# Optimization experiments

Hardware: AMD Instinct MI355X
Metric: run time of the kernel (lower is better)

Reference implementation:

```python
import jax, jax.numpy as jnp
import numpy as np

B, S, E, H = 8, 1024, 1024, 16
D = E // H  # per-head dim = 64
STD = 0.05  # nn.init.normal_ std used in the torch module


def setup_inputs() -> dict:
    key = jax.random.key(0)
    ks = jax.random.split(key, 9)
    inputs = jax.random.normal(ks[0], (B, S, E), dtype=jnp.float32)
    mlp_params_Q = jax.random.normal(ks[1], (B, E), dtype=jnp.float32)
    mlp_params_K = jax.random.normal(ks[2], (B, E), dtype=jnp.float32)
    W_Query = jax.random.normal(ks[3], (E, E), dtype=jnp.float32) * STD
    W_Key = jax.random.normal(ks[4], (E, E), dtype=jnp.float32) * STD
    W_Value = jax.random.normal(ks[5], (E, E), dtype=jnp.float32) * STD
    W_Out = jax.random.normal(ks[6], (E, E), dtype=jnp.float32) * STD  # nn.Linear weight [out, in]
    ln_gamma = jax.random.normal(ks[7], (E,), dtype=jnp.float32) * STD
    ln_beta = jax.random.normal(ks[8], (E,), dtype=jnp.float32) * STD
    return {"inputs": inputs, "mlp_params_Q": mlp_params_Q, "mlp_params_K": mlp_params_K,
            "W_Query": W_Query, "W_Key": W_Key, "W_Value": W_Value, "W_Out": W_Out,
            "ln_gamma": ln_gamma, "ln_beta": ln_beta}


def reference(inputs, mlp_params_Q, mlp_params_K, W_Query, W_Key, W_Value, W_Out, ln_gamma, ln_beta):
    # QKV projections: [B,S,E] @ [E,E]
    q = jnp.einsum('bse,ef->bsf', inputs, W_Query)
    k = jnp.einsum('bse,ef->bsf', inputs, W_Key)
    v = jnp.einsum('bse,ef->bsf', inputs, W_Value)
    # meta gate modulation (flag='gate', mode='QK'): per-batch channel gates, *2
    q = q * mlp_params_Q[:, None, :] * 2.0
    k = k * mlp_params_K[:, None, :] * 2.0
    # split heads: channels [h*D:(h+1)*D] -> head h (matches torch.split/stack)
    qh = q.reshape(B, S, H, D)
    kh = k.reshape(B, S, H, D)
    vh = v.reshape(B, S, H, D)
    # attention scores [B,H,S,S], scaled by sqrt(D)
    scores = jnp.einsum('bihd,bjhd->bhij', qh, kh) / jnp.sqrt(jnp.asarray(D, q.dtype))
    attn = jax.nn.softmax(scores, axis=-1)  # attn_dropout is identity at eval
    out = jnp.einsum('bhij,bjhd->bihd', attn, vh).reshape(B, S, E)  # concat heads
    # output projection (nn.Linear, no bias): x @ W.T; dropout identity at eval
    res = jnp.einsum('bse,fe->bsf', out, W_Out)
    # residual + LayerNorm(eps=1e-6)
    res = res + inputs
    mean = jnp.mean(res, axis=-1, keepdims=True)
    var = jnp.mean(jnp.square(res - mean), axis=-1, keepdims=True)
    res = (res - mean) * jax.lax.rsqrt(var + 1e-6) * ln_gamma + ln_beta
    return res
```

## Files before the change

kernel.cpp:

```cpp
#include <hip/hip_runtime.h>
#include <stdint.h>

#define Bn 8
#define Sn 1024
#define En 1024
#define Hn 16
#define Dn 64
#define Mn (Bn*Sn)

typedef unsigned short u16;
typedef _Float16 f16;
typedef _Float16 f16x8 __attribute__((ext_vector_type(8)));
typedef __fp16   h16x2 __attribute__((ext_vector_type(2)));
typedef float    f32x4 __attribute__((ext_vector_type(4)));

static __device__ __forceinline__ u16 f2h(float x){
  f16 h = (f16)x;
  union { f16 h; u16 u; } c; c.h = h; return c.u;
}
static __device__ __forceinline__ float h2f(u16 u){
  union { u16 u; f16 h; } c; c.u = u; return (float)c.h;
}
static __device__ __forceinline__ float fexp2(float x){
  float r; asm("v_exp_f32 %0, %1" : "=v"(r) : "v"(x)); return r;
}
static __device__ __forceinline__ f32x4 mfma16(f16x8 a, f16x8 b, f32x4 c){
  return __builtin_amdgcn_mfma_f32_16x16x32_f16(a, b, c, 0, 0, 0);
}
static __device__ __forceinline__ void gl_lds16(const u16* g, u16* l){
  __builtin_amdgcn_global_load_lds((__attribute__((address_space(1))) void*)g,
                                   (__attribute__((address_space(3))) void*)l, 16, 0, 0);
}

__global__ __launch_bounds__(256) void k_prep(const float* __restrict__ X,
    const float* __restrict__ Wq, const float* __restrict__ Wk,
    const float* __restrict__ Wv, const float* __restrict__ Wo,
    u16* __restrict__ xh, u16* __restrict__ wq, u16* __restrict__ wk,
    u16* __restrict__ wv, u16* __restrict__ wo){
  __shared__ float tsh[32][33];
  const int bid = blockIdx.x, tid = threadIdx.x;
  if (bid < 9216){
    const float* src = (bid < 8192) ? X : Wo;
    u16* dst = (bid < 8192) ? xh : wo;
    int i = (bid < 8192 ? bid : bid - 8192)*256 + tid;
    float4 v = ((const float4*)src)[i];
    ushort4 h; h.x = f2h(v.x); h.y = f2h(v.y); h.z = f2h(v.z); h.w = f2h(v.w);
    ((ushort4*)dst)[i] = h;
  } else {
    int pb = bid - 9216;
    int sel = pb >> 10, inner = pb & 1023;
    int bx = inner & 31, by = inner >> 5;
    int tx = tid & 31, ty = tid >> 5;
    const float* W = (sel == 0) ? Wq : (sel == 1) ? Wk : Wv;
    u16* D = (sel == 0) ? wq : (sel == 1) ? wk : wv;
    for (int i = 0; i < 32; i += 8)
      tsh[ty+i][tx] = W[(size_t)(by*32+ty+i)*En + bx*32+tx];
    __syncthreads();
    for (int i = 0; i < 32; i += 8)
      D[(size_t)(bx*32+ty+i)*En + by*32+tx] = f2h(tsh[tx][ty+i]);
  }
}

__global__ __launch_bounds__(256) void k_gemm_qkv(
    const u16* __restrict__ A, const u16* __restrict__ Bw,
    const float* __restrict__ gQ, const float* __restrict__ gK,
    u16* __restrict__ Cq, u16* __restrict__ Ck, u16* __restrict__ Vt){
  __shared__ u16 sA[2*128*32], sB[2*128*32];
  const int t = threadIdx.x, w = t >> 6, l = t & 63;
  const int lr = l & 15, lg = l >> 4;
  const int tn = blockIdx.x % 24, tm = blockIdx.x / 24;
  const int m0 = tm*128, n0 = tn*128;
  const int wr = (w >> 1)*64, wc = (w & 1)*64;
  f32x4 acc[4][4] = {};

#define GSTAGE(buf, k0_) do { \
    for (int c = 0; c < 2; c++){ \
      int ch  = c*256 + t; \
      int row = ch >> 2; \
      int xb  = (ch & 3) << 4; \
      int col = (k0_) + ((xb ^ ((row & 3) << 4)) >> 1); \
      int ldso = (buf)*8192 + (c*256 + w*64)*16; \
      gl_lds16(A  + (size_t)(m0+row)*En + col, (u16*)((char*)sA + ldso)); \
      gl_lds16(Bw + (size_t)(n0+row)*En + col, (u16*)((char*)sB + ldso)); \
    } } while (0)

  GSTAGE(0, 0);
  __syncthreads();
  for (int kt = 0; kt < En/32; kt++){
    const int cur = kt & 1;
    if (kt < En/32 - 1) GSTAGE(cur^1, (kt+1)*32);
    f16x8 af[4], bf[4];
    #pragma unroll
    for (int i = 0; i < 4; i++){
      int r  = wr + i*16 + lr;
      af[i] = *(const f16x8*)((const char*)sA + cur*8192 + r*64 + ((lg*16) ^ ((r & 3) << 4)));
      int n  = wc + i*16 + lr;
      bf[i] = *(const f16x8*)((const char*)sB + cur*8192 + n*64 + ((lg*16) ^ ((n & 3) << 4)));
    }
    __builtin_amdgcn_s_setprio(1);
    #pragma unroll
    for (int i = 0; i < 4; i++)
      #pragma unroll
      for (int j = 0; j < 4; j++)
        acc[i][j] = mfma16(af[i], bf[j], acc[i][j]);
    __builtin_amdgcn_s_setprio(0);
    __syncthreads();
  }
#undef GSTAGE
  const int bb = m0 >> 10;
  const int sel = n0 >> 10;
  if (sel < 2){
    const float* gate = sel ? gK : gQ;
    const float gs = sel ? 2.0f : 0.25f*1.4426950408889634f;
    u16* C = sel ? Ck : Cq;
    #pragma unroll
    for (int j = 0; j < 4; j++){
      int col = (n0 & 1023) + wc + j*16 + lr;
      float g = gate[bb*En + col] * gs;
      #pragma unroll
      for (int i = 0; i < 4; i++){
        int mbase = m0 + wr + i*16 + lg*4;
        #pragma unroll
        for (int r = 0; r < 4; r++)
          C[(size_t)(mbase + r)*En + col] = f2h(acc[i][j][r] * g);
      }
    }
  } else {
    const int s0 = (m0 & 1023) + wr;
    #pragma unroll
    for (int j = 0; j < 4; j++){
      int nn = (n0 - 2048) + wc + j*16 + lr;
      int hh = nn >> 6, d = nn & 63;
      u16* dst = Vt + ((size_t)(bb*Hn + hh)*Dn + d)*Sn;
      #pragma unroll
      for (int i = 0; i < 4; i++){
        int ss = s0 + i*16 + lg*4;
        ushort4 pk;
        pk.x = f2h(acc[i][j][0]); pk.y = f2h(acc[i][j][1]);
        pk.z = f2h(acc[i][j][2]); pk.w = f2h(acc[i][j][3]);
        *(ushort4*)&dst[ss] = pk;
      }
    }
  }
}

__global__ __launch_bounds__(256) void k_gemm_out(
    const u16* __restrict__ A, const u16* __restrict__ Bw,
    const float* __restrict__ resid, u16* __restrict__ resh){
  __shared__ u16 sA[2*128*32], sB[2*128*32];
  const int t = threadIdx.x, w = t >> 6, l = t & 63;
  const int lr = l & 15, lg = l >> 4;
  const int tn = blockIdx.x & 7, tm = blockIdx.x >> 3;
  const int m0 = tm*128, n0 = tn*128;
  const int wr = (w >> 1)*64, wc = (w & 1)*64;
  f32x4 acc[4][4] = {};

#define GSTAGE(buf, k0_) do { \
    for (int c = 0; c < 2; c++){ \
      int ch  = c*256 + t; \
      int row = ch >> 2; \
      int xb  = (ch & 3) << 4; \
      int col = (k0_) + ((xb ^ ((row & 3) << 4)) >> 1); \
      int ldso = (buf)*8192 + (c*256 + w*64)*16; \
      gl_lds16(A  + (size_t)(m0+row)*En + col, (u16*)((char*)sA + ldso)); \
      gl_lds16(Bw + (size_t)(n0+row)*En + col, (u16*)((char*)sB + ldso)); \
    } } while (0)

  GSTAGE(0, 0);
  __syncthreads();
  for (int kt = 0; kt < En/32; kt++){
    const int cur = kt & 1;
    if (kt < En/32 - 1) GSTAGE(cur^1, (kt+1)*32);
    f16x8 af[4], bf[4];
    #pragma unroll
    for (int i = 0; i < 4; i++){
      int r  = wr + i*16 + lr;
      af[i] = *(const f16x8*)((const char*)sA + cur*8192 + r*64 + ((lg*16) ^ ((r & 3) << 4)));
      int n  = wc + i*16 + lr;
      bf[i] = *(const f16x8*)((const char*)sB + cur*8192 + n*64 + ((lg*16) ^ ((n & 3) << 4)));
    }
    __builtin_amdgcn_s_setprio(1);
    #pragma unroll
    for (int i = 0; i < 4; i++)
      #pragma unroll
      for (int j = 0; j < 4; j++)
        acc[i][j] = mfma16(af[i], bf[j], acc[i][j]);
    __builtin_amdgcn_s_setprio(0);
    __syncthreads();
  }
#undef GSTAGE
  #pragma unroll
  for (int j = 0; j < 4; j++){
    int col = n0 + wc + j*16 + lr;
    #pragma unroll
    for (int i = 0; i < 4; i++){
      int mbase = m0 + wr + i*16 + lg*4;
      #pragma unroll
      for (int r = 0; r < 4; r++){
        size_t o = (size_t)(mbase + r)*En + col;
        resh[o] = f2h(acc[i][j][r] + resid[o]);
      }
    }
  }
}

__global__ __launch_bounds__(512) void k_attn(
    const u16* __restrict__ qp, const u16* __restrict__ kp,
    const u16* __restrict__ vt, u16* __restrict__ outp){
  __shared__ u16 sK[2][64*64];
  __shared__ u16 sVt[2][64*64];
  __shared__ u16 sP[8][16*72];
  const int t = threadIdx.x, w = t >> 6, l = t & 63;
  const int lr = l & 15, lg = l >> 4;
  const int qt = blockIdx.x >> 7, hb = blockIdx.x & 127;
  const int h = hb & 15, b = hb >> 4;
  const int q0 = qt*128 + w*16;

  const int srow = t >> 3, slot = t & 7, jc = slot ^ (srow & 7);
  const size_t gkbase = (size_t)(b*Sn + srow)*En + h*Dn + jc*8;
  const size_t gvbase = ((size_t)(b*Hn + h)*Dn + srow)*Sn + jc*8;

#define STAGE(buf, kt_) do { \
    gl_lds16(kp + gkbase + (size_t)(kt_)*64*En, (u16*)((char*)sK[buf] + w*1024)); \
    gl_lds16(vt + gvbase + (kt_)*64,            (u16*)((char*)sVt[buf] + w*1024)); \
  } while (0)

  size_t qrow = (size_t)(b*Sn + q0 + lr)*En + h*Dn;
  f16x8 qf[2];
  #pragma unroll
  for (int ks = 0; ks < 2; ks++)
    qf[ks] = *(const f16x8*)&qp[qrow + ks*32 + lg*8];
  f32x4 accO[4] = {};
  float mrun = -1e30f, lrun = 0.f;
  u16* P = &sP[w][0];

  STAGE(0, 0);
  __syncthreads();
  for (int kt = 0; kt < Sn/64; kt++){
    const int cur = kt & 1;
    if (kt < Sn/64 - 1) STAGE(cur^1, kt+1);
    f32x4 s[4] = {};
    __builtin_amdgcn_s_setprio(1);
    #pragma unroll
    for (int ks = 0; ks < 2; ks++)
      #pragma unroll
      for (int jt = 0; jt < 4; jt++){
        int j  = jt*16 + lr;
        int ob = j*128 + ((ks*64 + lg*16) ^ ((j & 7) << 4));
        f16x8 kf = *(const f16x8*)((const char*)sK[cur] + ob);
        s[jt] = mfma16(kf, qf[ks], s[jt]);
      }
    __builtin_amdgcn_s_setprio(0);
    float m16 = fmaxf(fmaxf(fmaxf(s[0][0], s[0][1]), fmaxf(s[0][2], s[0][3])),
                      fmaxf(fmaxf(s[1][0], s[1][1]), fmaxf(s[1][2], s[1][3])));
    m16 = fmaxf(m16, fmaxf(fmaxf(fmaxf(s[2][0], s[2][1]), fmaxf(s[2][2], s[2][3])),
                           fmaxf(fmaxf(s[3][0], s[3][1]), fmaxf(s[3][2], s[3][3]))));
    m16 = fmaxf(m16, __shfl_xor(m16, 16));
    m16 = fmaxf(m16, __shfl_xor(m16, 32));
    bool defer = __all(m16 <= mrun + 8.0f);
    float mn, sc;
    if (defer){ mn = mrun; sc = 1.0f; }
    else { mn = fmaxf(mrun, m16); sc = fexp2(mrun - mn); mrun = mn; }
    float ps = 0.f;
    #pragma unroll
    for (int jt = 0; jt < 4; jt++){
      float p0 = fexp2(s[jt][0] - mn), p1 = fexp2(s[jt][1] - mn);
      float p2 = fexp2(s[jt][2] - mn), p3 = fexp2(s[jt][3] - mn);
      ps += (p0 + p1) + (p2 + p3);
      union { h16x2 h; uint32_t u; } ca, cb;
      ca.h = __builtin_amdgcn_cvt_pkrtz(p0, p1);
      cb.h = __builtin_amdgcn_cvt_pkrtz(p2, p3);
      uint2 pk; pk.x = ca.u; pk.y = cb.u;
      *(uint2*)&P[lr*72 + jt*16 + lg*4] = pk;
    }
    ps += __shfl_xor(ps, 16);
    ps += __shfl_xor(ps, 32);
    lrun = lrun*sc + ps;
    if (!defer){
      #pragma unroll
      for (int r = 0; r < 4; r++){
        float scq = __shfl(sc, lg*4 + r);
        accO[0][r] *= scq; accO[1][r] *= scq;
        accO[2][r] *= scq; accO[3][r] *= scq;
      }
    }
    __builtin_amdgcn_s_setprio(1);
    #pragma unroll
    for (int js = 0; js < 2; js++){
      f16x8 pa = *(const f16x8*)&P[lr*72 + js*32 + lg*8];
      #pragma unroll
      for (int dt = 0; dt < 4; dt++){
        int d  = dt*16 + lr;
        int ob = d*128 + ((lg*16 + js*64) ^ ((d & 7) << 4));
        f16x8 vb = *(const f16x8*)((const char*)sVt[cur] + ob);
        accO[dt] = mfma16(pa, vb, accO[dt]);
      }
    }
    __builtin_amdgcn_s_setprio(0);
    __syncthreads();
  }
#undef STAGE
  float inv = 1.0f / lrun;
  float ir[4];
  #pragma unroll
  for (int r = 0; r < 4; r++) ir[r] = __shfl(inv, lg*4 + r);
  #pragma unroll
  for (int dt = 0; dt < 4; dt++){
    int dcol = h*Dn + dt*16 + lr;
    #pragma unroll
    for (int r = 0; r < 4; r++)
      outp[(size_t)(b*Sn + q0 + lg*4 + r)*En + dcol] = f2h(accO[dt][r] * ir[r]);
  }
}

__global__ __launch_bounds__(256) void k_ln(const u16* __restrict__ res,
    const float* __restrict__ gamma, const float* __restrict__ beta,
    float* __restrict__ out){
  int row = blockIdx.x, t = threadIdx.x;
  const u16* r = res + (size_t)row*En;
  ushort4 v4 = ((const ushort4*)r)[t];
  float vx = h2f(v4.x), vy = h2f(v4.y), vz = h2f(v4.z), vw = h2f(v4.w);
  float s = vx + vy + vz + vw;
  float q = vx*vx + vy*vy + vz*vz + vw*vw;
  for (int d = 1; d < 64; d <<= 1){ s += __shfl_xor(s, d); q += __shfl_xor(q, d); }
  __shared__ float ss[4], sq[4];
  int w = t >> 6, l = t & 63;
  if (l == 0){ ss[w] = s; sq[w] = q; }
  __syncthreads();
  s = ss[0] + ss[1] + ss[2] + ss[3];
  q = sq[0] + sq[1] + sq[2] + sq[3];
  float mean = s * (1.f/En);
  float var  = q * (1.f/En) - mean*mean;
  float rs   = rsqrtf(var + 1e-6f);
  float4 g = ((const float4*)gamma)[t], bb = ((const float4*)beta)[t];
  float4 o;
  o.x = (vx - mean)*rs*g.x + bb.x;
  o.y = (vy - mean)*rs*g.y + bb.y;
  o.z = (vz - mean)*rs*g.z + bb.z;
  o.w = (vw - mean)*rs*g.w + bb.w;
  ((float4*)(out + (size_t)row*En))[t] = o;
}

extern "C" void kernel_launch(void* const* d_in, const int* in_sizes, int n_in,
                              void* d_out, int out_size, void* d_ws, size_t ws_size,
                              hipStream_t stream){
  (void)in_sizes; (void)n_in; (void)out_size; (void)ws_size;
  const float* X     = (const float*)d_in[0];
  const float* gQ    = (const float*)d_in[1];
  const float* gK    = (const float*)d_in[2];
  const float* Wq    = (const float*)d_in[3];
  const float* Wk    = (const float*)d_in[4];
  const float* Wv    = (const float*)d_in[5];
  const float* Wo    = (const float*)d_in[6];
  const float* gamma = (const float*)d_in[7];
  const float* beta  = (const float*)d_in[8];
  float* out = (float*)d_out;

  char* ws = (char*)d_ws;
  const size_t sz = (size_t)Mn*En*2;
  u16* xh = (u16*)(ws + 0*sz);
  u16* qh = (u16*)(ws + 1*sz);
  u16* kh = (u16*)(ws + 2*sz);
  u16* vb = (u16*)(ws + 3*sz);
  u16* ao = (u16*)(ws + 4*sz);
  u16* res = (u16*)(ws + 0*sz);
  u16* wq = (u16*)(ws + 5*sz);
  u16* wk = wq + (size_t)En*En;
  u16* wv = wk + (size_t)En*En;
  u16* wo = wv + (size_t)En*En;

  k_prep<<<12288, 256, 0, stream>>>(X, Wq, Wk, Wv, Wo, xh, wq, wk, wv, wo);
  k_gemm_qkv<<<(Mn/128)*(3*En/128), 256, 0, stream>>>(xh, wq, gQ, gK, qh, kh, vb);
  k_attn<<<(Sn/128)*Hn*Bn, 512, 0, stream>>>(qh, kh, vb, ao);
  k_gemm_out<<<(Mn/128)*(En/128), 256, 0, stream>>>(ao, wo, X, res);
  k_ln<<<Mn, 256, 0, stream>>>(res, gamma, beta, out);
}
```

Measured before the change: 276.7 us.

## Double K tile to 64 in GEMMs and use explicit vmcnt waits with raw barriers

Result: faster. 263.6 us (-4.7%).

```diff
diff --git a/kernel.cpp b/kernel.cpp
--- a/kernel.cpp
+++ b/kernel.cpp
@@ -13,6 +13,9 @@
 typedef _Float16 f16x8 __attribute__((ext_vector_type(8)));
 typedef __fp16   h16x2 __attribute__((ext_vector_type(2)));
 typedef float    f32x4 __attribute__((ext_vector_type(4)));
+
+#define VMCNT(n) asm volatile("s_waitcnt vmcnt(" #n ")" ::: "memory")
+#define CFENCE() asm volatile("" ::: "memory")
 
 static __device__ __forceinline__ u16 f2h(float x){
   f16 h = (f16)x;
@@ -65,7 +68,7 @@
     const u16* __restrict__ A, const u16* __restrict__ Bw,
     const float* __restrict__ gQ, const float* __restrict__ gK,
     u16* __restrict__ Cq, u16* __restrict__ Ck, u16* __restrict__ Vt){
-  __shared__ u16 sA[2*128*32], sB[2*128*32];
+  __shared__ u16 sA[2*128*64], sB[2*128*64];
   const int t = threadIdx.x, w = t >> 6, l = t & 63;
   const int lr = l & 15, lg = l >> 4;
   const int tn = blockIdx.x % 24, tm = blockIdx.x / 24;
@@ -74,37 +77,42 @@
   f32x4 acc[4][4] = {};
 
 #define GSTAGE(buf, k0_) do { \
-    for (int c = 0; c < 2; c++){ \
+    for (int c = 0; c < 4; c++){ \
       int ch  = c*256 + t; \
-      int row = ch >> 2; \
-      int xb  = (ch & 3) << 4; \
-      int col = (k0_) + ((xb ^ ((row & 3) << 4)) >> 1); \
-      int ldso = (buf)*8192 + (c*256 + w*64)*16; \
-      gl_lds16(A  + (size_t)(m0+row)*En + col, (u16*)((char*)sA + ldso)); \
-      gl_lds16(Bw + (size_t)(n0+row)*En + col, (u16*)((char*)sB + ldso)); \
+      int row = ch >> 3; \
+      int jc  = (ch & 7) ^ (row & 7); \
+      int ldso = (buf)*16384 + (c*256 + w*64)*16; \
+      gl_lds16(A  + (size_t)(m0+row)*En + (k0_) + jc*8, (u16*)((char*)sA + ldso)); \
+      gl_lds16(Bw + (size_t)(n0+row)*En + (k0_) + jc*8, (u16*)((char*)sB + ldso)); \
     } } while (0)
 
   GSTAGE(0, 0);
-  __syncthreads();
-  for (int kt = 0; kt < En/32; kt++){
+  for (int kt = 0; kt < En/64; kt++){
     const int cur = kt & 1;
-    if (kt < En/32 - 1) GSTAGE(cur^1, (kt+1)*32);
-    f16x8 af[4], bf[4];
-    #pragma unroll
-    for (int i = 0; i < 4; i++){
-      int r  = wr + i*16 + lr;
-      af[i] = *(const f16x8*)((const char*)sA + cur*8192 + r*64 + ((lg*16) ^ ((r & 3) << 4)));
-      int n  = wc + i*16 + lr;
-      bf[i] = *(const f16x8*)((const char*)sB + cur*8192 + n*64 + ((lg*16) ^ ((n & 3) << 4)));
-    }
-    __builtin_amdgcn_s_setprio(1);
-    #pragma unroll
-    for (int i = 0; i < 4; i++)
-      #pragma unroll
-      for (int j = 0; j < 4; j++)
-        acc[i][j] = mfma16(af[i], bf[j], acc[i][j]);
-    __builtin_amdgcn_s_setprio(0);
-    __syncthreads();
+    if (kt < En/64 - 1){ GSTAGE(cur^1, (kt+1)*64); VMCNT(8); }
+    else               { VMCNT(0); }
+    __builtin_amdgcn_s_barrier();
+    CFENCE();
+    #pragma unroll
+    for (int ks = 0; ks < 2; ks++){
+      f16x8 af[4], bf[4];
+      #pragma unroll
+      for (int i = 0; i < 4; i++){
+        int r  = wr + i*16 + lr;
+        af[i] = *(const f16x8*)((const char*)sA + cur*16384 + r*128 + ((ks*64 + lg*16) ^ ((r & 7) << 4)));
+        int n  = wc + i*16 + lr;
+        bf[i] = *(const f16x8*)((const char*)sB + cur*16384 + n*128 + ((ks*64 + lg*16) ^ ((n & 7) << 4)));
+      }
+      __builtin_amdgcn_s_setprio(1);
+      #pragma unroll
+      for (int i = 0; i < 4; i++)
+        #pragma unroll
+        for (int j = 0; j < 4; j++)
+          acc[i][j] = mfma16(af[i], bf[j], acc[i][j]);
+      __builtin_amdgcn_s_setprio(0);
+    }
+    CFENCE();
+    __builtin_amdgcn_s_barrier();
   }
 #undef GSTAGE
   const int bb = m0 >> 10;
@@ -147,7 +155,7 @@
 __global__ __launch_bounds__(256) void k_gemm_out(
     const u16* __restrict__ A, const u16* __restrict__ Bw,
     const float* __restrict__ resid, u16* __restrict__ resh){
-  __shared__ u16 sA[2*128*32], sB[2*128*32];
+  __shared__ u16 sA[2*128*64], sB[2*128*64];
   const int t = threadIdx.x, w = t >> 6, l = t & 63;
   const int lr = l & 15, lg = l >> 4;
   const int tn = blockIdx.x & 7, tm = blockIdx.x >> 3;
@@ -156,37 +164,42 @@
   f32x4 acc[4][4] = {};
 
 #define GSTAGE(buf, k0_) do { \
-    for (int c = 0; c < 2; c++){ \
+    for (int c = 0; c < 4; c++){ \
       int ch  = c*256 + t; \
-      int row = ch >> 2; \
-      int xb  = (ch & 3) << 4; \
-      int col = (k0_) + ((xb ^ ((row & 3) << 4)) >> 1); \
-      int ldso = (buf)*8192 + (c*256 + w*64)*16; \
-      gl_lds16(A  + (size_t)(m0+row)*En + col, (u16*)((char*)sA + ldso)); \
-      gl_lds16(Bw + (size_t)(n0+row)*En + col, (u16*)((char*)sB + ldso)); \
+      int row = ch >> 3; \
+      int jc  = (ch & 7) ^ (row & 7); \
+      int ldso = (buf)*16384 + (c*256 + w*64)*16; \
+      gl_lds16(A  + (size_t)(m0+row)*En + (k0_) + jc*8, (u16*)((char*)sA + ldso)); \
+      gl_lds16(Bw + (size_t)(n0+row)*En + (k0_) + jc*8, (u16*)((char*)sB + ldso)); \
     } } while (0)
 
   GSTAGE(0, 0);
-  __syncthreads();
-  for (int kt = 0; kt < En/32; kt++){
+  for (int kt = 0; kt < En/64; kt++){
     const int cur = kt & 1;
-    if (kt < En/32 - 1) GSTAGE(cur^1, (kt+1)*32);
-    f16x8 af[4], bf[4];
-    #pragma unroll
-    for (int i = 0; i < 4; i++){
-      int r  = wr + i*16 + lr;
-      af[i] = *(const f16x8*)((const char*)sA + cur*8192 + r*64 + ((lg*16) ^ ((r & 3) << 4)));
-      int n  = wc + i*16 + lr;
-      bf[i] = *(const f16x8*)((const char*)sB + cur*8192 + n*64 + ((lg*16) ^ ((n & 3) << 4)));
-    }
-    __builtin_amdgcn_s_setprio(1);
-    #pragma unroll
-    for (int i = 0; i < 4; i++)
-      #pragma unroll
-      for (int j = 0; j < 4; j++)
-        acc[i][j] = mfma16(af[i], bf[j], acc[i][j]);
-    __builtin_amdgcn_s_setprio(0);
-    __syncthreads();
+    if (kt < En/64 - 1){ GSTAGE(cur^1, (kt+1)*64); VMCNT(8); }
+    else               { VMCNT(0); }
+    __builtin_amdgcn_s_barrier();
+    CFENCE();
+    #pragma unroll
+    for (int ks = 0; ks < 2; ks++){
+      f16x8 af[4], bf[4];
+      #pragma unroll
+      for (int i = 0; i < 4; i++){
+        int r  = wr + i*16 + lr;
+        af[i] = *(const f16x8*)((const char*)sA + cur*16384 + r*128 + ((ks*64 + lg*16) ^ ((r & 7) << 4)));
+        int n  = wc + i*16 + lr;
+        bf[i] = *(const f16x8*)((const char*)sB + cur*16384 + n*128 + ((ks*64 + lg*16) ^ ((n & 7) << 4)));
+      }
+      __builtin_amdgcn_s_setprio(1);
+      #pragma unroll
+      for (int i = 0; i < 4; i++)
+        #pragma unroll
+        for (int j = 0; j < 4; j++)
+          acc[i][j] = mfma16(af[i], bf[j], acc[i][j]);
+      __builtin_amdgcn_s_setprio(0);
+    }
+    CFENCE();
+    __builtin_amdgcn_s_barrier();
   }
 #undef GSTAGE
   #pragma unroll
```
